# Kernel tuning notes

Hardware: AMD Instinct MI355X
Metric: run time of the kernel (lower is better)

## Reference

```python
import jax, jax.numpy as jnp
import numpy as np

N_NODES = 50000
N_EDGES = 1600000
IN_CH = 32
HID = 64
K = 2


def _dconv(X, edge_index, edge_weight, W, b):
    """Diffusion graph conv (torch_geometric_temporal DConv, K=2).

    X: [N, C_in], W: [2, K, C_in, C_out], b: [C_out].
    Direction 0: forward transition P_f = D_out^{-1} A  (applied as P_f^T X).
    Direction 1: backward transition P_b = D_in^{-1} A^T (applied as P_b^T X).
    """
    n = X.shape[0]
    row, col = edge_index[0], edge_index[1]
    deg_out = jax.ops.segment_sum(edge_weight, row, num_segments=n)  # out-degree (row sums of A)
    deg_in = jax.ops.segment_sum(edge_weight, col, num_segments=n)   # in-degree  (col sums of A)
    norm_out = edge_weight / deg_out[row]  # [E]
    norm_in = edge_weight / deg_in[col]    # [E]

    # k = 0 term: identity for both directions
    H = X @ (W[0, 0] + W[1, 0])

    # k = 1 term: one diffusion step in each direction
    # forward dir: out[i] = sum_{(j->i)} w/deg_out[j] * X[j]
    Tx_o = jax.ops.segment_sum(norm_out[:, None] * X[row], col, num_segments=n)
    # backward dir: out[i] = sum_{(i->j)} w/deg_in[j] * X[j]
    Tx_i = jax.ops.segment_sum(norm_in[:, None] * X[col], row, num_segments=n)
    H = H + Tx_o @ W[0, 1] + Tx_i @ W[1, 1]
    return H + b


def setup_inputs() -> dict:
    key = jax.random.key(0)
    ks = jax.random.split(key, 12)
    cat_ch = IN_CH + HID  # GRU concatenates [X, H]
    s = 1.0 / np.sqrt(cat_ch)
    inp = {
        "x": jax.random.normal(ks[0], (N_NODES, IN_CH), dtype=jnp.float32),
        "edge_index": jax.random.randint(ks[1], (2, N_EDGES), 0, N_NODES, dtype=jnp.int32),
        "edge_weight": jax.random.uniform(ks[2], (N_EDGES,), dtype=jnp.float32, minval=0.05, maxval=1.0),
        "Wz": jax.random.uniform(ks[3], (2, K, cat_ch, HID), dtype=jnp.float32, minval=-s, maxval=s),
        "bz": jnp.zeros((HID,), dtype=jnp.float32),
        "Wr": jax.random.uniform(ks[4], (2, K, cat_ch, HID), dtype=jnp.float32, minval=-s, maxval=s),
        "br": jnp.zeros((HID,), dtype=jnp.float32),
        "Wh": jax.random.uniform(ks[5], (2, K, cat_ch, HID), dtype=jnp.float32, minval=-s, maxval=s),
        "bh": jnp.zeros((HID,), dtype=jnp.float32),
        "Wlin": jax.random.uniform(ks[6], (HID, 1), dtype=jnp.float32, minval=-1.0 / np.sqrt(HID), maxval=1.0 / np.sqrt(HID)),
        "blin": jnp.zeros((1,), dtype=jnp.float32),
    }
    return inp


def reference(x, edge_index, edge_weight, Wz, bz, Wr, br, Wh, bh, Wlin, blin):
    n = x.shape[0]
    H0 = jnp.zeros((n, HID), dtype=x.dtype)  # initial hidden state (H=None)
    XH = jnp.concatenate([x, H0], axis=-1)   # [N, IN_CH+HID]
    Z = jax.nn.sigmoid(_dconv(XH, edge_index, edge_weight, Wz, bz))
    R = jax.nn.sigmoid(_dconv(XH, edge_index, edge_weight, Wr, br))
    XHR = jnp.concatenate([x, H0 * R], axis=-1)
    H_tilde = jnp.tanh(_dconv(XHR, edge_index, edge_weight, Wh, bh))
    H = Z * H0 + (1.0 - Z) * H_tilde
    out = jnp.maximum(H, 0.0) @ Wlin + blin  # ReLU then Linear(hidden, 1)
    return out
```

## Files before the change

### kernel.cpp

```cpp
#include <hip/hip_runtime.h>
#include <math.h>

#define N_NODES 50000
#define N_EDGES 1600000
#define IN_CH 32
#define HID 64

#define NBIN 782
#define BIN_SHIFT 6
#define CHUNK 8192
#define NCHK ((N_EDGES + CHUNK - 1) / CHUNK)
#define FG_CAP 2560

#define PREP_WPREP_BLOCKS 48
#define PREP_XCONV_BLOCKS ((N_NODES * 8 + 255) / 256)
#define PREP_BLOCKS (PREP_WPREP_BLOCKS + PREP_XCONV_BLOCKS + 1)

#define WS_WBF      0
#define WS_BINTOT   6144
#define WS_BINCNT   7712
#define WS_XSB      107808
#define WS_TXO      907808
#define WS_TXI      1707808
#define WS_XSO      2507808
#define WS_XSI      3307808
#define WS_BINNED   4107808
#define WS_END      12115488

typedef __attribute__((ext_vector_type(8))) short bf16x8;
typedef __attribute__((ext_vector_type(4))) float f32x4;

__device__ __forceinline__ unsigned short f2bf(float f) {
    unsigned int u = __float_as_uint(f);
    return (unsigned short)((u + 0x7fffu + ((u >> 16) & 1u)) >> 16);
}
__device__ __forceinline__ float bf2f(unsigned short b) {
    return __uint_as_float((unsigned int)b << 16);
}
__device__ __forceinline__ float bflo(int u) {
    return __uint_as_float(((unsigned int)u) << 16);
}
__device__ __forceinline__ float bfhi(int u) {
    return __uint_as_float(((unsigned int)u) & 0xffff0000u);
}

__global__ __launch_bounds__(256) void prep_kernel(
    const float* __restrict__ Wz, const float* __restrict__ Wh,
    const float4* __restrict__ x4, unsigned short* __restrict__ wbf,
    ushort4* __restrict__ xsb, int* __restrict__ binTot) {
    int tid = threadIdx.x;
    int b = blockIdx.x;
    if (b < PREP_WPREP_BLOCKS) {
        int idx = b * 256 + tid;
        if (idx >= 12288) return;
        int j = idx & 7, ln = (idx >> 3) & 63, bn = (idx >> 9) & 7, kk = idx >> 12;
        int k = kk * 32 + (ln >> 4) * 8 + j;
        int n = bn * 16 + (ln & 15);
        int slab = k >> 5, c = k & 31;
        const float* W = (n < 64) ? Wz : Wh;
        int o = n & 63;
        float v;
        if (slab == 0)      v = W[c * 64 + o] + W[(2 * 96 + c) * 64 + o];
        else if (slab == 1) v = W[(96 + c) * 64 + o];
        else                v = W[(3 * 96 + c) * 64 + o];
        wbf[idx] = f2bf(v);
    } else if (b < PREP_WPREP_BLOCKS + PREP_XCONV_BLOCKS) {
        int i = (b - PREP_WPREP_BLOCKS) * 256 + tid;
        if (i >= N_NODES * 8) return;
        float4 v = x4[i];
        ushort4 o;
        o.x = f2bf(v.x); o.y = f2bf(v.y); o.z = f2bf(v.z); o.w = f2bf(v.w);
        xsb[i] = o;
    } else {
        for (int i = tid; i < 1568; i += 256) binTot[i] = 0;
    }
}

__global__ __launch_bounds__(512) void partition_kernel(
    const int* __restrict__ ei, const float* __restrict__ ew,
    int* __restrict__ binTot, int2* __restrict__ binned) {
    __shared__ int2 stg[CHUNK];
    __shared__ int hist[NBIN];
    __shared__ int lst[NBIN];
    __shared__ int gBase[NBIN];
    __shared__ int sc[512];
    int tid = threadIdx.x;
    int dir = (blockIdx.x >= NCHK) ? 1 : 0;
    int chunk = blockIdx.x - dir * NCHK;

    for (int i = tid; i < NBIN; i += 512) hist[i] = 0;
    __syncthreads();

    int e0 = chunk * CHUNK;
    int n_e = min(CHUNK, N_EDGES - e0);
    int binv[16], rankv[16];
    int2 pay[16];
#pragma unroll
    for (int j = 0; j < 16; ++j) {
        int idx = tid + j * 512;
        if (idx < n_e) {
            int e = e0 + idx;
            int r = ei[e];
            int c = ei[N_EDGES + e];
            int dst = dir ? r : c;
            int src = dir ? c : r;
            int b = dst >> BIN_SHIFT;
            binv[j] = b;
            rankv[j] = atomicAdd(&hist[b], 1);
            pay[j] = make_int2((int)(((unsigned)b << 22) | ((unsigned)(dst & 63) << 16) |
                                     (unsigned)src),
                               __float_as_int(ew[e]));
        } else {
            binv[j] = -1;
        }
    }
    __syncthreads();
    int ps = (tid < 391) ? (hist[2 * tid] + hist[2 * tid + 1]) : 0;
    sc[tid] = ps;
    __syncthreads();
    for (int off = 1; off < 512; off <<= 1) {
        int u = (tid >= off) ? sc[tid - off] : 0;
        __syncthreads();
        sc[tid] += u;
        __syncthreads();
    }
    if (tid < 391) {
        int pref = sc[tid] - ps;
        lst[2 * tid] = pref;
        lst[2 * tid + 1] = pref + hist[2 * tid];
    }
    for (int i = tid; i < NBIN; i += 512)
        gBase[i] = (hist[i] > 0) ? atomicAdd(&binTot[dir * NBIN + i], hist[i]) : 0;
    __syncthreads();
#pragma unroll
    for (int j = 0; j < 16; ++j)
        if (binv[j] >= 0) stg[lst[binv[j]] + rankv[j]] = pay[j];
    __syncthreads();
    for (int p = tid; p < n_e; p += 512) {
        int2 v2 = stg[p];
        int b = (int)(((unsigned)v2.x) >> 22);
        int off = gBase[b] + (p - lst[b]);
        if (off < FG_CAP)
            binned[(dir * NBIN + b) * FG_CAP + off] =
                make_int2(v2.x & 0x3FFFFF, v2.y);
    }
}

__global__ __launch_bounds__(256) void bindeg_kernel(
    const int* __restrict__ binTot, const int2* __restrict__ binned,
    const float4* __restrict__ x4, int* __restrict__ binCnt,
    ushort4* __restrict__ xso, ushort4* __restrict__ xsi) {
    __shared__ float wsum[64];
    __shared__ int cnt[64];
    int tid = threadIdx.x;
    int b = blockIdx.x;
    int dir = (b >= NBIN) ? 1 : 0;
    if (tid < 64) { wsum[tid] = 0.f; cnt[tid] = 0; }
    __syncthreads();
    int lo = b * FG_CAP;
    int n_e = min(binTot[b], FG_CAP);
    for (int p = tid; p < n_e; p += 256) {
        int2 v = binned[lo + p];
        int d = v.x >> 16;
        atomicAdd(&cnt[d], 1);
        atomicAdd(&wsum[d], __int_as_float(v.y));
    }
    __syncthreads();
    if (tid < 64) {
        binCnt[b * 64 + tid] = cnt[tid];
        float s = wsum[tid];
        wsum[tid] = (s != 0.f) ? (1.f / s) : 0.f;
    }
    __syncthreads();
    ushort4* xsd = dir ? xso : xsi;
    int node0 = (b - dir * NBIN) * 64;
#pragma unroll
    for (int i = tid; i < 512; i += 256) {
        int nl = i >> 3, q = i & 7;
        int node = node0 + nl;
        if (node < N_NODES) {
            float4 v = x4[node * 8 + q];
            float r = wsum[nl];
            ushort4 o;
            o.x = f2bf(v.x * r); o.y = f2bf(v.y * r);
            o.z = f2bf(v.z * r); o.w = f2bf(v.w * r);
            xsd[node * 8 + q] = o;
        }
    }
}

__global__ __launch_bounds__(256, 7) void fgather_kernel(
    const int4* __restrict__ xso4, const int4* __restrict__ xsi4,
    const int* __restrict__ binTot, const int* __restrict__ binCnt,
    const int2* __restrict__ binned, float* __restrict__ ws_f) {
    __shared__ int2 s_edge[FG_CAP];
    __shared__ int s_off[65];
    __shared__ int s_cur[64];
    __shared__ int sc[64];
    int tid = threadIdx.x;
    int b = blockIdx.x;
    int dir = (b >= NBIN) ? 1 : 0;
    int bin = b - dir * NBIN;

    int v = (tid < 64) ? binCnt[b * 64 + tid] : 0;
    if (tid < 64) sc[tid] = v;
    __syncthreads();
    for (int off = 1; off < 64; off <<= 1) {
        int u = (tid < 64 && tid >= off) ? sc[tid - off] : 0;
        __syncthreads();
        if (tid < 64) sc[tid] += u;
        __syncthreads();
    }
    if (tid < 64) {
        s_off[tid] = sc[tid] - v;
        s_cur[tid] = sc[tid] - v;
    }
    if (tid == 63) s_off[64] = sc[63];
    __syncthreads();

    int n_e = min(binTot[b], FG_CAP);
    const int2* bb = binned + b * FG_CAP;
    for (int base = 0; base < n_e; base += 2048) {
        int2 ev[8];
#pragma unroll
        for (int j = 0; j < 8; ++j) {
            int idx = base + j * 256 + tid;
            if (idx < n_e) ev[j] = bb[idx];
        }
#pragma unroll
        for (int j = 0; j < 8; ++j) {
            int idx = base + j * 256 + tid;
            if (idx < n_e) {
                int rk = atomicAdd(&s_cur[ev[j].x >> 16], 1);
                if (rk < FG_CAP)
                    s_edge[rk] = make_int2(ev[j].x & 0xffff, ev[j].y);
            }
        }
    }
    __syncthreads();

    const int4* xsrc = dir ? xsi4 : xso4;
    int4* outp = (int4*)(ws_f + (dir == 0 ? WS_TXO : WS_TXI));
    int lane = tid & 3;
    int nl = tid >> 2;
    int p = s_off[nl], end = s_off[nl + 1];
    float acc[8];
#pragma unroll
    for (int j = 0; j < 8; ++j) acc[j] = 0.f;
    for (; p + 3 < end; p += 4) {
        int2 v0 = s_edge[p], v1 = s_edge[p + 1];
        int2 v2 = s_edge[p + 2], v3 = s_edge[p + 3];
        int4 a0 = xsrc[v0.x * 4 + lane];
        int4 a1 = xsrc[v1.x * 4 + lane];
        int4 a2 = xsrc[v2.x * 4 + lane];
        int4 a3 = xsrc[v3.x * 4 + lane];
        float c0 = __int_as_float(v0.y), c1 = __int_as_float(v1.y);
        float c2 = __int_as_float(v2.y), c3 = __int_as_float(v3.y);
        acc[0] += c0 * bflo(a0.x) + c1 * bflo(a1.x) + c2 * bflo(a2.x) + c3 * bflo(a3.x);
        acc[1] += c0 * bfhi(a0.x) + c1 * bfhi(a1.x) + c2 * bfhi(a2.x) + c3 * bfhi(a3.x);
        acc[2] += c0 * bflo(a0.y) + c1 * bflo(a1.y) + c2 * bflo(a2.y) + c3 * bflo(a3.y);
        acc[3] += c0 * bfhi(a0.y) + c1 * bfhi(a1.y) + c2 * bfhi(a2.y) + c3 * bfhi(a3.y);
        acc[4] += c0 * bflo(a0.z) + c1 * bflo(a1.z) + c2 * bflo(a2.z) + c3 * bflo(a3.z);
        acc[5] += c0 * bfhi(a0.z) + c1 * bfhi(a1.z) + c2 * bfhi(a2.z) + c3 * bfhi(a3.z);
        acc[6] += c0 * bflo(a0.w) + c1 * bflo(a1.w) + c2 * bflo(a2.w) + c3 * bflo(a3.w);
        acc[7] += c0 * bfhi(a0.w) + c1 * bfhi(a1.w) + c2 * bfhi(a2.w) + c3 * bfhi(a3.w);
    }
    for (; p < end; ++p) {
        int2 v0 = s_edge[p];
        float c0 = __int_as_float(v0.y);
        int4 a = xsrc[v0.x * 4 + lane];
        acc[0] += c0 * bflo(a.x);
        acc[1] += c0 * bfhi(a.x);
        acc[2] += c0 * bflo(a.y);
        acc[3] += c0 * bfhi(a.y);
        acc[4] += c0 * bflo(a.z);
        acc[5] += c0 * bfhi(a.z);
        acc[6] += c0 * bflo(a.w);
        acc[7] += c0 * bfhi(a.w);
    }
    int node = bin * 64 + nl;
    if (node < N_NODES) {
        int4 o;
        o.x = (int)f2bf(acc[0]) | ((int)f2bf(acc[1]) << 16);
        o.y = (int)f2bf(acc[2]) | ((int)f2bf(acc[3]) << 16);
        o.z = (int)f2bf(acc[4]) | ((int)f2bf(acc[5]) << 16);
        o.w = (int)f2bf(acc[6]) | ((int)f2bf(acc[7]) << 16);
        outp[node * 4 + lane] = o;
    }
}

#define DN_GROUP 64
#define DN_BLOCKS ((N_NODES + DN_GROUP - 1) / DN_GROUP)
__global__ __launch_bounds__(256) void dense_kernel(
    const int4* __restrict__ xsb4,
    const int4* __restrict__ txo_b, const int4* __restrict__ txi_b,
    const unsigned short* __restrict__ wbf,
    const float* __restrict__ bz, const float* __restrict__ bh,
    const float* __restrict__ Wlin, const float* __restrict__ blin,
    float* __restrict__ out) {
    __shared__ unsigned short sA[64 * 104];
    __shared__ unsigned short sB[12288];

    int tid = threadIdx.x;
    int lane = tid & 63, w = tid >> 6;
    int lm = lane & 15, quad = lane >> 4;

    for (int idx = tid; idx < 3072; idx += 256)
        *(ushort4*)&sB[idx * 4] = ((const ushort4*)wbf)[idx];

    int node0 = blockIdx.x * DN_GROUP;
    for (int idx = tid; idx < 64 * 4; idx += 256) {
        int nl = idx >> 2, q = idx & 3;
        int node = node0 + nl;
        int4 v = (node < N_NODES) ? xsb4[node * 4 + q] : make_int4(0, 0, 0, 0);
        *(int4*)&sA[nl * 104 + q * 8] = v;
    }
    for (int idx = tid; idx < 64 * 8; idx += 256) {
        int nl = idx >> 3, q = idx & 7;
        int node = node0 + nl;
        int4 v = make_int4(0, 0, 0, 0);
        if (node < N_NODES)
            v = (q < 4) ? txo_b[node * 4 + q] : txi_b[node * 4 + (q - 4)];
        *(int4*)&sA[nl * 104 + 32 + q * 8] = v;
    }

    float bzv[4], bhv[4], wlv[4];
#pragma unroll
    for (int bn = 0; bn < 4; ++bn) {
        int o = lm + 16 * bn;
        bzv[bn] = bz[o]; bhv[bn] = bh[o]; wlv[bn] = Wlin[o];
    }
    float bl = blin[0];
    __syncthreads();

    f32x4 acc[8];
#pragma unroll
    for (int bn = 0; bn < 4; ++bn) {
        acc[bn]     = (f32x4){bzv[bn], bzv[bn], bzv[bn], bzv[bn]};
        acc[bn + 4] = (f32x4){bhv[bn], bhv[bn], bhv[bn], bhv[bn]};
    }
#pragma unroll
    for (int kk = 0; kk < 3; ++kk) {
        bf16x8 af = *(const bf16x8*)&sA[(w * 16 + lm) * 104 + kk * 32 + quad * 8];
#pragma unroll
        for (int bn = 0; bn < 8; ++bn) {
            bf16x8 bf = *(const bf16x8*)&sB[((kk * 8 + bn) * 64 + lane) * 8];
            acc[bn] = __builtin_amdgcn_mfma_f32_16x16x32_bf16(af, bf, acc[bn], 0, 0, 0);
        }
    }

    float partial[4] = {0.f, 0.f, 0.f, 0.f};
#pragma unroll
    for (int bn = 0; bn < 4; ++bn) {
#pragma unroll
        for (int reg = 0; reg < 4; ++reg) {
            float az = acc[bn][reg], ah = acc[bn + 4][reg];
            float z = 1.f / (1.f + __expf(-az));
            float ht = 1.f - 2.f / (__expf(2.f * ah) + 1.f);
            partial[reg] += fmaxf((1.f - z) * ht, 0.f) * wlv[bn];
        }
    }
#pragma unroll
    for (int reg = 0; reg < 4; ++reg) {
        float s = partial[reg];
        s += __shfl_xor(s, 1, 64);
        s += __shfl_xor(s, 2, 64);
        s += __shfl_xor(s, 4, 64);
        s += __shfl_xor(s, 8, 64);
        if (lm == 0) {
            int node = node0 + w * 16 + quad * 4 + reg;
            if (node < N_NODES) out[node] = s + bl;
        }
    }
}

extern "C" void kernel_launch(void* const* d_in, const int* in_sizes, int n_in,
                              void* d_out, int out_size, void* d_ws, size_t ws_size,
                              hipStream_t stream) {
    const float* x = (const float*)d_in[0];
    const int* ei = (const int*)d_in[1];
    const float* ew = (const float*)d_in[2];
    const float* Wz = (const float*)d_in[3];
    const float* bz = (const float*)d_in[4];
    const float* Wh = (const float*)d_in[7];
    const float* bh = (const float*)d_in[8];
    const float* Wlin = (const float*)d_in[9];
    const float* blin = (const float*)d_in[10];
    float* out = (float*)d_out;
    float* wf = (float*)d_ws;
    int* wi = (int*)d_ws;
    int2* binned = (int2*)(wi + WS_BINNED);

    prep_kernel<<<PREP_BLOCKS, 256, 0, stream>>>(
        Wz, Wh, (const float4*)x, (unsigned short*)(wi + WS_WBF),
        (ushort4*)(wi + WS_XSB), wi + WS_BINTOT);
    partition_kernel<<<2 * NCHK, 512, 0, stream>>>(ei, ew, wi + WS_BINTOT, binned);
    bindeg_kernel<<<2 * NBIN, 256, 0, stream>>>(
        wi + WS_BINTOT, binned, (const float4*)x, wi + WS_BINCNT,
        (ushort4*)(wi + WS_XSO), (ushort4*)(wi + WS_XSI));
    fgather_kernel<<<2 * NBIN, 256, 0, stream>>>(
        (const int4*)(wi + WS_XSO), (const int4*)(wi + WS_XSI),
        wi + WS_BINTOT, wi + WS_BINCNT, binned, wf);
    dense_kernel<<<DN_BLOCKS, 256, 0, stream>>>(
        (const int4*)(wi + WS_XSB), (const int4*)(wi + WS_TXO),
        (const int4*)(wi + WS_TXI), (const unsigned short*)(wi + WS_WBF),
        bz, bh, Wlin, blin, out);
}
```

Before: 168.4 us.

## Fuse gather with dense GEMM and partition both directions per edge chunk

The gather and dense kernels become one kernel. Each block gathers both diffusion directions for its 64-node bin into shared memory and then runs the MFMA dense stage directly, so the Tx_o/Tx_i buffers never round-trip through global memory. The partition kernel now loads each edge chunk once and bins it for both directions, and the chunk size is halved to keep the grid size up. The cost is fewer gather blocks (one per bin instead of two), a lower occupancy bound, and shared memory reused between the edge list and the weights.

```diff
diff --git a/kernel.cpp b/kernel.cpp
--- a/kernel.cpp
+++ b/kernel.cpp
@@ -8,7 +8,7 @@
 
 #define NBIN 782
 #define BIN_SHIFT 6
-#define CHUNK 8192
+#define CHUNK 4096
 #define NCHK ((N_EDGES + CHUNK - 1) / CHUNK)
 #define FG_CAP 2560
 
@@ -20,12 +20,10 @@
 #define WS_BINTOT   6144
 #define WS_BINCNT   7712
 #define WS_XSB      107808
-#define WS_TXO      907808
-#define WS_TXI      1707808
-#define WS_XSO      2507808
-#define WS_XSI      3307808
-#define WS_BINNED   4107808
-#define WS_END      12115488
+#define WS_XSO      907808
+#define WS_XSI      1707808
+#define WS_BINNED   2507808
+#define WS_END      10515488
 
 typedef __attribute__((ext_vector_type(8))) short bf16x8;
 typedef __attribute__((ext_vector_type(4))) float f32x4;
@@ -85,64 +83,77 @@
     __shared__ int gBase[NBIN];
     __shared__ int sc[512];
     int tid = threadIdx.x;
-    int dir = (blockIdx.x >= NCHK) ? 1 : 0;
-    int chunk = blockIdx.x - dir * NCHK;
-
-    for (int i = tid; i < NBIN; i += 512) hist[i] = 0;
-    __syncthreads();
+    int chunk = blockIdx.x;
 
     int e0 = chunk * CHUNK;
     int n_e = min(CHUNK, N_EDGES - e0);
-    int binv[16], rankv[16];
-    int2 pay[16];
-#pragma unroll
-    for (int j = 0; j < 16; ++j) {
+    int rr[8], cc[8];
+    float wwv[8];
+#pragma unroll
+    for (int j = 0; j < 8; ++j) {
         int idx = tid + j * 512;
         if (idx < n_e) {
             int e = e0 + idx;
-            int r = ei[e];
-            int c = ei[N_EDGES + e];
-            int dst = dir ? r : c;
-            int src = dir ? c : r;
-            int b = dst >> BIN_SHIFT;
-            binv[j] = b;
-            rankv[j] = atomicAdd(&hist[b], 1);
-            pay[j] = make_int2((int)(((unsigned)b << 22) | ((unsigned)(dst & 63) << 16) |
-                                     (unsigned)src),
-                               __float_as_int(ew[e]));
+            rr[j] = ei[e];
+            cc[j] = ei[N_EDGES + e];
+            wwv[j] = ew[e];
         } else {
-            binv[j] = -1;
-        }
-    }
-    __syncthreads();
-    int ps = (tid < 391) ? (hist[2 * tid] + hist[2 * tid + 1]) : 0;
-    sc[tid] = ps;
-    __syncthreads();
-    for (int off = 1; off < 512; off <<= 1) {
-        int u = (tid >= off) ? sc[tid - off] : 0;
-        __syncthreads();
-        sc[tid] += u;
-        __syncthreads();
-    }
-    if (tid < 391) {
-        int pref = sc[tid] - ps;
-        lst[2 * tid] = pref;
-        lst[2 * tid + 1] = pref + hist[2 * tid];
-    }
-    for (int i = tid; i < NBIN; i += 512)
-        gBase[i] = (hist[i] > 0) ? atomicAdd(&binTot[dir * NBIN + i], hist[i]) : 0;
-    __syncthreads();
-#pragma unroll
-    for (int j = 0; j < 16; ++j)
-        if (binv[j] >= 0) stg[lst[binv[j]] + rankv[j]] = pay[j];
-    __syncthreads();
-    for (int p = tid; p < n_e; p += 512) {
-        int2 v2 = stg[p];
-        int b = (int)(((unsigned)v2.x) >> 22);
-        int off = gBase[b] + (p - lst[b]);
-        if (off < FG_CAP)
-            binned[(dir * NBIN + b) * FG_CAP + off] =
-                make_int2(v2.x & 0x3FFFFF, v2.y);
+            rr[j] = -1;
+        }
+    }
+
+    for (int dir = 0; dir < 2; ++dir) {
+        for (int i = tid; i < NBIN; i += 512) hist[i] = 0;
+        __syncthreads();
+        int binv[8], rankv[8];
+        int2 pay[8];
+#pragma unroll
+        for (int j = 0; j < 8; ++j) {
+            if (rr[j] >= 0) {
+                int dst = dir ? rr[j] : cc[j];
+                int src = dir ? cc[j] : rr[j];
+                int b = dst >> BIN_SHIFT;
+                binv[j] = b;
+                rankv[j] = atomicAdd(&hist[b], 1);
+                pay[j] = make_int2(
+                    (int)(((unsigned)b << 22) | ((unsigned)(dst & 63) << 16) |
+                          (unsigned)src),
+                    __float_as_int(wwv[j]));
+            } else {
+                binv[j] = -1;
+            }
+        }
+        __syncthreads();
+        int ps = (tid < 391) ? (hist[2 * tid] + hist[2 * tid + 1]) : 0;
+        sc[tid] = ps;
+        __syncthreads();
+        for (int off = 1; off < 512; off <<= 1) {
+            int u = (tid >= off) ? sc[tid - off] : 0;
+            __syncthreads();
+            sc[tid] += u;
+            __syncthreads();
+        }
+        if (tid < 391) {
+            int pref = sc[tid] - ps;
+            lst[2 * tid] = pref;
+            lst[2 * tid + 1] = pref + hist[2 * tid];
+        }
+        for (int i = tid; i < NBIN; i += 512)
+            gBase[i] = (hist[i] > 0) ? atomicAdd(&binTot[dir * NBIN + i], hist[i]) : 0;
+        __syncthreads();
+#pragma unroll
+        for (int j = 0; j < 8; ++j)
+            if (binv[j] >= 0) stg[lst[binv[j]] + rankv[j]] = pay[j];
+        __syncthreads();
+        for (int p = tid; p < n_e; p += 512) {
+            int2 v2 = stg[p];
+            int b = (int)(((unsigned)v2.x) >> 22);
+            int off = gBase[b] + (p - lst[b]);
+            if (off < FG_CAP)
+                binned[(dir * NBIN + b) * FG_CAP + off] =
+                    make_int2(v2.x & 0x3FFFFF, v2.y);
+        }
+        __syncthreads();
     }
 }
 
@@ -189,148 +200,129 @@
     }
 }
 
-__global__ __launch_bounds__(256, 7) void fgather_kernel(
+__global__ __launch_bounds__(256, 4) void fgdense_kernel(
     const int4* __restrict__ xso4, const int4* __restrict__ xsi4,
-    const int* __restrict__ binTot, const int* __restrict__ binCnt,
-    const int2* __restrict__ binned, float* __restrict__ ws_f) {
-    __shared__ int2 s_edge[FG_CAP];
+    const int4* __restrict__ xsb4, const int* __restrict__ binTot,
+    const int* __restrict__ binCnt, const int2* __restrict__ binned,
+    const unsigned short* __restrict__ wbf,
+    const float* __restrict__ bz, const float* __restrict__ bh,
+    const float* __restrict__ Wlin, const float* __restrict__ blin,
+    float* __restrict__ out) {
+    __shared__ __align__(16) unsigned short sA[64 * 104];
+    __shared__ __align__(16) char s_u[24576];
     __shared__ int s_off[65];
     __shared__ int s_cur[64];
     __shared__ int sc[64];
+    int2* s_edge = (int2*)s_u;
+    unsigned short* sB = (unsigned short*)s_u;
+
     int tid = threadIdx.x;
-    int b = blockIdx.x;
-    int dir = (b >= NBIN) ? 1 : 0;
-    int bin = b - dir * NBIN;
-
-    int v = (tid < 64) ? binCnt[b * 64 + tid] : 0;
-    if (tid < 64) sc[tid] = v;
-    __syncthreads();
-    for (int off = 1; off < 64; off <<= 1) {
-        int u = (tid < 64 && tid >= off) ? sc[tid - off] : 0;
-        __syncthreads();
-        if (tid < 64) sc[tid] += u;
-        __syncthreads();
-    }
-    if (tid < 64) {
-        s_off[tid] = sc[tid] - v;
-        s_cur[tid] = sc[tid] - v;
-    }
-    if (tid == 63) s_off[64] = sc[63];
-    __syncthreads();
-
-    int n_e = min(binTot[b], FG_CAP);
-    const int2* bb = binned + b * FG_CAP;
-    for (int base = 0; base < n_e; base += 2048) {
-        int2 ev[8];
-#pragma unroll
-        for (int j = 0; j < 8; ++j) {
-            int idx = base + j * 256 + tid;
-            if (idx < n_e) ev[j] = bb[idx];
-        }
-#pragma unroll
-        for (int j = 0; j < 8; ++j) {
-            int idx = base + j * 256 + tid;
-            if (idx < n_e) {
-                int rk = atomicAdd(&s_cur[ev[j].x >> 16], 1);
-                if (rk < FG_CAP)
-                    s_edge[rk] = make_int2(ev[j].x & 0xffff, ev[j].y);
+    int bin = blockIdx.x;
+    int lane4 = tid & 3, nl = tid >> 2;
+    int lane = tid & 63, w = tid >> 6;
+    int lm = lane & 15, quad = lane >> 4;
+    int node0 = bin * 64;
+
+    {
+        int n_ = tid >> 2, q = tid & 3;
+        int node = node0 + n_;
+        int4 v = (node < N_NODES) ? xsb4[node * 4 + q] : make_int4(0, 0, 0, 0);
+        *(int4*)&sA[n_ * 104 + q * 8] = v;
+    }
+    float bzv[4], bhv[4], wlv[4];
+#pragma unroll
+    for (int bn = 0; bn < 4; ++bn) {
+        int o = lm + 16 * bn;
+        bzv[bn] = bz[o]; bhv[bn] = bh[o]; wlv[bn] = Wlin[o];
+    }
+    float bl = blin[0];
+
+    for (int dir = 0; dir < 2; ++dir) {
+        int b = dir * NBIN + bin;
+        int v = (tid < 64) ? binCnt[b * 64 + tid] : 0;
+        if (tid < 64) sc[tid] = v;
+        __syncthreads();
+        for (int off = 1; off < 64; off <<= 1) {
+            int u = (tid < 64 && tid >= off) ? sc[tid - off] : 0;
+            __syncthreads();
+            if (tid < 64) sc[tid] += u;
+            __syncthreads();
+        }
+        if (tid < 64) {
+            s_off[tid] = sc[tid] - v;
+            s_cur[tid] = sc[tid] - v;
+        }
+        if (tid == 63) s_off[64] = sc[63];
+        __syncthreads();
+
+        int n_e = min(binTot[b], FG_CAP);
+        const int2* bb = binned + b * FG_CAP;
+        for (int base = 0; base < n_e; base += 2048) {
+            int2 ev[8];
+#pragma unroll
+            for (int j = 0; j < 8; ++j) {
+                int idx = base + j * 256 + tid;
+                if (idx < n_e) ev[j] = bb[idx];
             }
-        }
-    }
-    __syncthreads();
-
-    const int4* xsrc = dir ? xsi4 : xso4;
-    int4* outp = (int4*)(ws_f + (dir == 0 ? WS_TXO : WS_TXI));
-    int lane = tid & 3;
-    int nl = tid >> 2;
-    int p = s_off[nl], end = s_off[nl + 1];
-    float acc[8];
-#pragma unroll
-    for (int j = 0; j < 8; ++j) acc[j] = 0.f;
-    for (; p + 3 < end; p += 4) {
-        int2 v0 = s_edge[p], v1 = s_edge[p + 1];
-        int2 v2 = s_edge[p + 2], v3 = s_edge[p + 3];
-        int4 a0 = xsrc[v0.x * 4 + lane];
-        int4 a1 = xsrc[v1.x * 4 + lane];
-        int4 a2 = xsrc[v2.x * 4 + lane];
-        int4 a3 = xsrc[v3.x * 4 + lane];
-        float c0 = __int_as_float(v0.y), c1 = __int_as_float(v1.y);
-        float c2 = __int_as_float(v2.y), c3 = __int_as_float(v3.y);
-        acc[0] += c0 * bflo(a0.x) + c1 * bflo(a1.x) + c2 * bflo(a2.x) + c3 * bflo(a3.x);
-        acc[1] += c0 * bfhi(a0.x) + c1 * bfhi(a1.x) + c2 * bfhi(a2.x) + c3 * bfhi(a3.x);
-        acc[2] += c0 * bflo(a0.y) + c1 * bflo(a1.y) + c2 * bflo(a2.y) + c3 * bflo(a3.y);
-        acc[3] += c0 * bfhi(a0.y) + c1 * bfhi(a1.y) + c2 * bfhi(a2.y) + c3 * bfhi(a3.y);
-        acc[4] += c0 * bflo(a0.z) + c1 * bflo(a1.z) + c2 * bflo(a2.z) + c3 * bflo(a3.z);
-        acc[5] += c0 * bfhi(a0.z) + c1 * bfhi(a1.z) + c2 * bfhi(a2.z) + c3 * bfhi(a3.z);
-        acc[6] += c0 * bflo(a0.w) + c1 * bflo(a1.w) + c2 * bflo(a2.w) + c3 * bflo(a3.w);
-        acc[7] += c0 * bfhi(a0.w) + c1 * bfhi(a1.w) + c2 * bfhi(a2.w) + c3 * bfhi(a3.w);
-    }
-    for (; p < end; ++p) {
-        int2 v0 = s_edge[p];
-        float c0 = __int_as_float(v0.y);
-        int4 a = xsrc[v0.x * 4 + lane];
-        acc[0] += c0 * bflo(a.x);
-        acc[1] += c0 * bfhi(a.x);
-        acc[2] += c0 * bflo(a.y);
-        acc[3] += c0 * bfhi(a.y);
-        acc[4] += c0 * bflo(a.z);
-        acc[5] += c0 * bfhi(a.z);
-        acc[6] += c0 * bflo(a.w);
-        acc[7] += c0 * bfhi(a.w);
-    }
-    int node = bin * 64 + nl;
-    if (node < N_NODES) {
+#pragma unroll
+            for (int j = 0; j < 8; ++j) {
+                int idx = base + j * 256 + tid;
+                if (idx < n_e) {
+                    int rk = atomicAdd(&s_cur[ev[j].x >> 16], 1);
+                    if (rk < FG_CAP)
+                        s_edge[rk] = make_int2(ev[j].x & 0xffff, ev[j].y);
+                }
+            }
+        }
+        __syncthreads();
+
+        const int4* xsrc = dir ? xsi4 : xso4;
+        int p = s_off[nl], end = s_off[nl + 1];
+        float acc[8];
+#pragma unroll
+        for (int j = 0; j < 8; ++j) acc[j] = 0.f;
+        for (; p + 3 < end; p += 4) {
+            int2 v0 = s_edge[p], v1 = s_edge[p + 1];
+            int2 v2 = s_edge[p + 2], v3 = s_edge[p + 3];
+            int4 a0 = xsrc[v0.x * 4 + lane4];
+            int4 a1 = xsrc[v1.x * 4 + lane4];
+            int4 a2 = xsrc[v2.x * 4 + lane4];
+            int4 a3 = xsrc[v3.x * 4 + lane4];
+            float c0 = __int_as_float(v0.y), c1 = __int_as_float(v1.y);
+            float c2 = __int_as_float(v2.y), c3 = __int_as_float(v3.y);
+            acc[0] += c0 * bflo(a0.x) + c1 * bflo(a1.x) + c2 * bflo(a2.x) + c3 * bflo(a3.x);
+            acc[1] += c0 * bfhi(a0.x) + c1 * bfhi(a1.x) + c2 * bfhi(a2.x) + c3 * bfhi(a3.x);
+            acc[2] += c0 * bflo(a0.y) + c1 * bflo(a1.y) + c2 * bflo(a2.y) + c3 * bflo(a3.y);
+            acc[3] += c0 * bfhi(a0.y) + c1 * bfhi(a1.y) + c2 * bfhi(a2.y) + c3 * bfhi(a3.y);
+            acc[4] += c0 * bflo(a0.z) + c1 * bflo(a1.z) + c2 * bflo(a2.z) + c3 * bflo(a3.z);
+            acc[5] += c0 * bfhi(a0.z) + c1 * bfhi(a1.z) + c2 * bfhi(a2.z) + c3 * bfhi(a3.z);
+            acc[6] += c0 * bflo(a0.w) + c1 * bflo(a1.w) + c2 * bflo(a2.w) + c3 * bflo(a3.w);
+            acc[7] += c0 * bfhi(a0.w) + c1 * bfhi(a1.w) + c2 * bfhi(a2.w) + c3 * bfhi(a3.w);
+        }
+        for (; p < end; ++p) {
+            int2 v0 = s_edge[p];
+            float c0 = __int_as_float(v0.y);
+            int4 a = xsrc[v0.x * 4 + lane4];
+            acc[0] += c0 * bflo(a.x);
+            acc[1] += c0 * bfhi(a.x);
+            acc[2] += c0 * bflo(a.y);
+            acc[3] += c0 * bfhi(a.y);
+            acc[4] += c0 * bflo(a.z);
+            acc[5] += c0 * bfhi(a.z);
+            acc[6] += c0 * bflo(a.w);
+            acc[7] += c0 * bfhi(a.w);
+        }
         int4 o;
         o.x = (int)f2bf(acc[0]) | ((int)f2bf(acc[1]) << 16);
         o.y = (int)f2bf(acc[2]) | ((int)f2bf(acc[3]) << 16);
         o.z = (int)f2bf(acc[4]) | ((int)f2bf(acc[5]) << 16);
         o.w = (int)f2bf(acc[6]) | ((int)f2bf(acc[7]) << 16);
-        outp[node * 4 + lane] = o;
-    }
-}
-
-#define DN_GROUP 64
-#define DN_BLOCKS ((N_NODES + DN_GROUP - 1) / DN_GROUP)
-__global__ __launch_bounds__(256) void dense_kernel(
-    const int4* __restrict__ xsb4,
-    const int4* __restrict__ txo_b, const int4* __restrict__ txi_b,
-    const unsigned short* __restrict__ wbf,
-    const float* __restrict__ bz, const float* __restrict__ bh,
-    const float* __restrict__ Wlin, const float* __restrict__ blin,
-    float* __restrict__ out) {
-    __shared__ unsigned short sA[64 * 104];
-    __shared__ unsigned short sB[12288];
-
-    int tid = threadIdx.x;
-    int lane = tid & 63, w = tid >> 6;
-    int lm = lane & 15, quad = lane >> 4;
+        *(int4*)&sA[nl * 104 + 32 + dir * 32 + lane4 * 8] = o;
+        __syncthreads();
+    }
 
     for (int idx = tid; idx < 3072; idx += 256)
         *(ushort4*)&sB[idx * 4] = ((const ushort4*)wbf)[idx];
-
-    int node0 = blockIdx.x * DN_GROUP;
-    for (int idx = tid; idx < 64 * 4; idx += 256) {
-        int nl = idx >> 2, q = idx & 3;
-        int node = node0 + nl;
-        int4 v = (node < N_NODES) ? xsb4[node * 4 + q] : make_int4(0, 0, 0, 0);
-        *(int4*)&sA[nl * 104 + q * 8] = v;
-    }
-    for (int idx = tid; idx < 64 * 8; idx += 256) {
-        int nl = idx >> 3, q = idx & 7;
-        int node = node0 + nl;
-        int4 v = make_int4(0, 0, 0, 0);
-        if (node < N_NODES)
-            v = (q < 4) ? txo_b[node * 4 + q] : txi_b[node * 4 + (q - 4)];
-        *(int4*)&sA[nl * 104 + 32 + q * 8] = v;
-    }
-
-    float bzv[4], bhv[4], wlv[4];
-#pragma unroll
-    for (int bn = 0; bn < 4; ++bn) {
-        int o = lm + 16 * bn;
-        bzv[bn] = bz[o]; bhv[bn] = bh[o]; wlv[bn] = Wlin[o];
-    }
-    float bl = blin[0];
     __syncthreads();
 
     f32x4 acc[8];
@@ -387,22 +379,18 @@
     const float* Wlin = (const float*)d_in[9];
     const float* blin = (const float*)d_in[10];
     float* out = (float*)d_out;
-    float* wf = (float*)d_ws;
     int* wi = (int*)d_ws;
     int2* binned = (int2*)(wi + WS_BINNED);
 
     prep_kernel<<<PREP_BLOCKS, 256, 0, stream>>>(
         Wz, Wh, (const float4*)x, (unsigned short*)(wi + WS_WBF),
         (ushort4*)(wi + WS_XSB), wi + WS_BINTOT);
-    partition_kernel<<<2 * NCHK, 512, 0, stream>>>(ei, ew, wi + WS_BINTOT, binned);
+    partition_kernel<<<NCHK, 512, 0, stream>>>(ei, ew, wi + WS_BINTOT, binned);
     bindeg_kernel<<<2 * NBIN, 256, 0, stream>>>(
         wi + WS_BINTOT, binned, (const float4*)x, wi + WS_BINCNT,
         (ushort4*)(wi + WS_XSO), (ushort4*)(wi + WS_XSI));
-    fgather_kernel<<<2 * NBIN, 256, 0, stream>>>(
+    fgdense_kernel<<<NBIN, 256, 0, stream>>>(
         (const int4*)(wi + WS_XSO), (const int4*)(wi + WS_XSI),
-        wi + WS_BINTOT, wi + WS_BINCNT, binned, wf);
-    dense_kernel<<<DN_BLOCKS, 256, 0, stream>>>(
-        (const int4*)(wi + WS_XSB), (const int4*)(wi + WS_TXO),
-        (const int4*)(wi + WS_TXI), (const unsigned short*)(wi + WS_WBF),
-        bz, bh, Wlin, blin, out);
-}
+        (const int4*)(wi + WS_XSB), wi + WS_BINTOT, wi + WS_BINCNT, binned,
+        (const unsigned short*)(wi + WS_WBF), bz, bh, Wlin, blin, out);
+}
```

After: 173.2 us. 2.9% more time.
